# Kernel optimization log

Hardware: AMD Instinct MI355X
Metric: run time of the kernel (lower is better)

Reference implementation:

```python
import jax, jax.numpy as jnp
import numpy as np

N_NODES = 50000
N_EDGES = 1600000
N_GRAPHS = 1000
F_IN = 92      # atom_input_features
WIDTH = 128    # config.width
F_OUT = 64     # output_features
LENGTHSCALE = 8.0  # config.edge_lengthscale


def setup_inputs() -> dict:
    key = jax.random.key(0)
    ks = jax.random.split(key, 12)
    inp = {
        "atom_features": jax.random.normal(ks[0], (N_NODES, F_IN), dtype=jnp.float32),
        "bondlength": jax.random.normal(ks[1], (N_EDGES, 3), dtype=jnp.float32) * 2.0,
        "src": jax.random.randint(ks[2], (N_EDGES,), 0, N_NODES, dtype=jnp.int32),
        "dst": jax.random.randint(ks[3], (N_EDGES,), 0, N_NODES, dtype=jnp.int32),
        "graph_ids": jnp.sort(jax.random.randint(ks[4], (N_NODES,), 0, N_GRAPHS, dtype=jnp.int32)),
        # atom_embedding Linear(F_IN, WIDTH)
        "W0": jax.random.normal(ks[5], (F_IN, WIDTH), dtype=jnp.float32) * 0.05,
        "b0": jnp.zeros((WIDTH,), dtype=jnp.float32),
        # GraphConv layer1 (WIDTH -> WIDTH)
        "W1": jax.random.normal(ks[6], (WIDTH, WIDTH), dtype=jnp.float32) * 0.05,
        "b1": jnp.zeros((WIDTH,), dtype=jnp.float32),
        # GraphConv layer2 (WIDTH -> F_OUT)
        "W2": jax.random.normal(ks[7], (WIDTH, F_OUT), dtype=jnp.float32) * 0.05,
        "b2": jnp.zeros((F_OUT,), dtype=jnp.float32),
    }
    return inp


def _degrees(src, dst, n_nodes):
    ones = jnp.ones(src.shape[0], dtype=jnp.float32)
    out_deg = jax.ops.segment_sum(ones, src, num_segments=n_nodes)
    in_deg = jax.ops.segment_sum(ones, dst, num_segments=n_nodes)
    # DGL GraphConv clamps degrees to min 1 (norm='both')
    return jnp.clip(out_deg, 1.0, None), jnp.clip(in_deg, 1.0, None)


def reference(atom_features, bondlength, src, dst, graph_ids, W0, b0, W1, b1, W2, b2):
    # edge weights: exp(-|r|^2 / lengthscale^2)
    r2 = jnp.sum(bondlength * bondlength, axis=1)  # [E]
    ew = jnp.exp(-r2 / (LENGTHSCALE ** 2))         # [E]

    out_deg, in_deg = _degrees(src, dst, N_NODES)
    norm_src = out_deg ** -0.5  # [N]
    norm_dst = in_deg ** -0.5   # [N]

    # atom embedding
    h = atom_features @ W0 + b0  # [N, WIDTH]

    # GraphConv layer1 (in==out: aggregate then weight), norm='both'
    hs = h * norm_src[:, None]
    m = hs[src] * ew[:, None]                                   # [E, WIDTH]
    agg = jax.ops.segment_sum(m, dst, num_segments=N_NODES)
    x = agg * norm_dst[:, None]
    x = jax.nn.relu(x @ W1 + b1)

    # GraphConv layer2 (in > out: weight first, then aggregate)
    hs = (x * norm_src[:, None]) @ W2                           # [N, F_OUT]
    m = hs[src] * ew[:, None]                                   # [E, F_OUT]
    agg = jax.ops.segment_sum(m, dst, num_segments=N_NODES)
    x = agg * norm_dst[:, None] + b2

    # AvgPooling readout per graph
    cnt = jnp.clip(jax.ops.segment_sum(jnp.ones(N_NODES, jnp.float32), graph_ids, num_segments=N_GRAPHS), 1.0, None)
    pooled = jax.ops.segment_sum(x, graph_ids, num_segments=N_GRAPHS) / cnt[:, None]
    return jnp.squeeze(pooled)  # [N_GRAPHS, F_OUT]
```

## Files before the change

### kernel.cpp

```cpp
#include <hip/hip_runtime.h>
#include <hip/hip_fp16.h>

#define N_NODES  50000
#define N_EDGES  1600000
#define N_GRAPHS 1000
#define F_IN     92
#define WIDTH    128
#define F_OUT    64
#define CHUNK    16384
#define NBLK_E   98
#define HPB      25024
#define HWRD     6256
#define XPITCH   48
#define BKT      196
#define CAP      9216
#define BINCHUNK 4096
#define NBIN     391

static const size_t CURS  = 0;
static const size_t CSRB  = 256;
static const size_t NSRC  = 520;
static const size_t NDST  = 50520;
static const size_t SVAL  = 100520;
static const size_t ROWP  = 150520;
static const size_t HSR   = 200528;
static const size_t SGW   = 813616;
static const size_t SGB   = 2619952;
static const size_t CSR   = 3071536;
static const size_t XB    = 4671536;
static const size_t W01   = 7071536;
static const size_t BW1   = 7083312;
static const size_t W01P  = 7083440;
static const size_t W2P   = 7089584;
static const size_t GAGG  = 7093680;
static const size_t HS2   = 11893680;
static const size_t AGG2  = GAGG;

typedef __attribute__((ext_vector_type(8))) _Float16 half8v;
typedef __attribute__((ext_vector_type(4))) float f32x4;

__device__ inline unsigned short f2bf(float f) {
    unsigned u = __float_as_uint(f);
    return (unsigned short)((u + 0x7fff + ((u >> 16) & 1)) >> 16);
}
__device__ inline float bflo(unsigned u) { return __uint_as_float(u << 16); }
__device__ inline float bfhi(unsigned u) { return __uint_as_float(u & 0xffff0000u); }
__device__ inline unsigned short f2h(float f) {
    return __half_as_ushort(__float2half(f));
}
__device__ inline float csr_w(unsigned v) {
    return __half2float(__ushort_as_half((unsigned short)(v >> 16)));
}

__global__ void k_init(unsigned* __restrict__ cursor) {
    cursor[threadIdx.x] = (unsigned)threadIdx.x * CAP;
}

__global__ __launch_bounds__(256) void k_srcHist(const int* __restrict__ src,
                                                 unsigned char* __restrict__ h_src) {
    __shared__ unsigned sh[HWRD];
    const int e0 = blockIdx.x * CHUNK;
    const int ecnt = min(CHUNK, N_EDGES - e0);
    for (int i = threadIdx.x; i < HWRD; i += 256) sh[i] = 0;
    __syncthreads();
    for (int i = threadIdx.x; i < ecnt; i += 256) {
        int v = src[e0 + i];
        atomicAdd(&sh[v >> 3], 1u << ((v & 7) * 4));
    }
    __syncthreads();
    unsigned* out = (unsigned*)(h_src + (size_t)blockIdx.x * HPB);
    for (int i = threadIdx.x; i < HWRD; i += 256) out[i] = sh[i];
}

__global__ __launch_bounds__(256) void k_nsrc(const unsigned char* __restrict__ h_src,
                                              float* __restrict__ nsrc) {
    int n = blockIdx.x * 256 + threadIdx.x;
    if (n >= N_NODES) return;
    const int byte = n >> 1, shn = (n & 1) * 4;
    unsigned so = 0;
    for (int b = 0; b < NBLK_E; ++b)
        so += (h_src[(size_t)b * HPB + byte] >> shn) & 0xfu;
    nsrc[n] = rsqrtf((float)max(so, 1u));
}

__global__ void k_packX(const float* __restrict__ af, unsigned* __restrict__ xb) {
    int idx = blockIdx.x * blockDim.x + threadIdx.x;
    if (idx >= N_NODES * XPITCH) return;
    int n = idx / XPITCH, c = idx - n * XPITCH;
    unsigned v = 0;
    if (c < 46) {
        const float* p = af + (size_t)n * F_IN + 2 * c;
        v = (unsigned)f2bf(p[0]) | ((unsigned)f2bf(p[1]) << 16);
    }
    xb[idx] = v;
}

__global__ __launch_bounds__(256) void k_bin(const float* __restrict__ bl,
                                             const int* __restrict__ src,
                                             const int* __restrict__ dst,
                                             const float* __restrict__ nsrc,
                                             unsigned* __restrict__ cursor,
                                             unsigned* __restrict__ sgw,
                                             unsigned char* __restrict__ sgb) {
    __shared__ unsigned hcnt[256];
    __shared__ unsigned gbase[256];
    const int t = threadIdx.x;
    const int e0 = blockIdx.x * BINCHUNK;
    hcnt[t] = 0;
    __syncthreads();
    unsigned entry[16], meta[16];
#pragma unroll
    for (int i = 0; i < 16; ++i) {
        int e = e0 + t + i * 256;
        meta[i] = 0xFFFFFFFFu;
        if (e < N_EDGES) {
            float x = bl[3 * e], y = bl[3 * e + 1], z = bl[3 * e + 2];
            int s = src[e], d = dst[e];
            float w = expf(-(x * x + y * y + z * z) * (1.0f / 64.0f)) * nsrc[s];
            entry[i] = (unsigned)s | ((unsigned)f2h(w) << 16);
            int bkt = d >> 8;
            unsigned r = atomicAdd(&hcnt[bkt], 1u);
            meta[i] = ((unsigned)bkt << 20) | ((unsigned)(d & 255) << 12) | r;
        }
    }
    __syncthreads();
    if (t < BKT) gbase[t] = hcnt[t] ? atomicAdd(&cursor[t], hcnt[t]) : 0u;
    __syncthreads();
#pragma unroll
    for (int i = 0; i < 16; ++i) {
        if (meta[i] != 0xFFFFFFFFu) {
            unsigned bkt = meta[i] >> 20;
            unsigned slot = gbase[bkt] + (meta[i] & 0xFFFu);
            if (slot < (bkt + 1) * CAP) {
                sgw[slot] = entry[i];
                sgb[slot] = (unsigned char)((meta[i] >> 12) & 0xFFu);
            }
        }
    }
}

__global__ __launch_bounds__(256) void k_bscan(const unsigned* __restrict__ cursor,
                                               int* __restrict__ csrb,
                                               int* __restrict__ rowp) {
    __shared__ int sd[256];
    const int t = threadIdx.x;
    int c = (t < BKT) ? (int)(cursor[t] - (unsigned)t * CAP) : 0;
    sd[t] = c;
    __syncthreads();
    for (int off = 1; off < 256; off <<= 1) {
        int v = (t >= off) ? sd[t - off] : 0;
        __syncthreads();
        sd[t] += v;
        __syncthreads();
    }
    if (t < BKT) csrb[t] = sd[t] - c;
    if (t == 0) rowp[N_NODES] = N_EDGES;
}

__global__ __launch_bounds__(256) void k_csr(const unsigned* __restrict__ cursor,
                                             const int* __restrict__ csrb,
                                             const unsigned* __restrict__ sgw,
                                             const unsigned char* __restrict__ sgb,
                                             unsigned* __restrict__ csr,
                                             int* __restrict__ rowp,
                                             float* __restrict__ ndst) {
    __shared__ unsigned se[CAP];
    __shared__ unsigned char sd8[CAP];
    __shared__ unsigned dh[256];
    __shared__ unsigned dcur[256];
    __shared__ int sscan[256];
    const int b = blockIdx.x, t = threadIdx.x;
    const int cnt = (int)(cursor[b] - (unsigned)b * CAP);
    const int base = csrb[b];
    for (int i = t; i < cnt; i += 256) {
        se[i] = sgw[(size_t)b * CAP + i];
        sd8[i] = sgb[(size_t)b * CAP + i];
    }
    dh[t] = 0;
    __syncthreads();
    for (int i = t; i < cnt; i += 256) atomicAdd(&dh[sd8[i]], 1u);
    __syncthreads();
    int v = (int)dh[t];
    sscan[t] = v;
    __syncthreads();
    for (int off = 1; off < 256; off <<= 1) {
        int a = (t >= off) ? sscan[t - off] : 0;
        __syncthreads();
        sscan[t] += a;
        __syncthreads();
    }
    dcur[t] = (unsigned)(sscan[t] - v);
    const int node = b * 256 + t;
    if (node < N_NODES) {
        rowp[node] = base + (sscan[t] - v);
        ndst[node] = rsqrtf((float)max((unsigned)v, 1u));
    }
    __syncthreads();
    for (int i = t; i < cnt; i += 256) {
        unsigned pos = atomicAdd(&dcur[sd8[i]], 1u);
        csr[(size_t)base + pos] = se[i];
    }
}

__global__ __launch_bounds__(128) void k_w01(const float* __restrict__ W0,
                                             const float* __restrict__ W1,
                                             const float* __restrict__ b0,
                                             float* __restrict__ w01,
                                             float* __restrict__ bw1) {
    const int t = threadIdx.x;
    const int k = blockIdx.x;
    float acc = 0.0f;
    if (k < F_IN) {
        for (int j = 0; j < WIDTH; ++j)
            acc = fmaf(W0[k * WIDTH + j], W1[j * WIDTH + t], acc);
        w01[k * WIDTH + t] = acc;
    } else {
        for (int j = 0; j < WIDTH; ++j)
            acc = fmaf(b0[j], W1[j * WIDTH + t], acc);
        bw1[t] = acc;
    }
}

__global__ __launch_bounds__(256) void k_prepW(const float* __restrict__ w01,
                                               const float* __restrict__ W2,
                                               unsigned* __restrict__ w01p,
                                               unsigned* __restrict__ w2p) {
    int idx = blockIdx.x * 256 + threadIdx.x;
    if (idx < 6144) {
        int q = idx & 3, lane = (idx >> 2) & 63;
        int rest = idx >> 8;
        int kb = rest % 3, t = rest / 3;
        int k = kb * 32 + ((lane >> 4) * 8) + 2 * q;
        int n = t * 16 + (lane & 15);
        float lo = (k < F_IN) ? w01[k * WIDTH + n] : 0.f;
        float hi = (k + 1 < F_IN) ? w01[(k + 1) * WIDTH + n] : 0.f;
        w01p[idx] = (unsigned)f2h(lo) | ((unsigned)f2h(hi) << 16);
    } else if (idx < 10240) {
        int i2 = idx - 6144;
        int q = i2 & 3, lane = (i2 >> 2) & 63;
        int rest = i2 >> 8;
        int kb = rest & 3, t = rest >> 2;
        int k = kb * 32 + ((lane >> 4) * 8) + 2 * q;
        int n = t * 16 + (lane & 15);
        float lo = W2[k * F_OUT + n];
        float hi = W2[(k + 1) * F_OUT + n];
        w2p[i2] = (unsigned)f2h(lo) | ((unsigned)f2h(hi) << 16);
    }
}

__global__ __launch_bounds__(256) void k_gatherG(const int* __restrict__ rowp,
                                                 const unsigned* __restrict__ csr,
                                                 const unsigned* __restrict__ xb,
                                                 float2* __restrict__ gf2,
                                                 float* __restrict__ S) {
    __shared__ unsigned sb[4][64];
    const int wid = threadIdx.x >> 6;
    const int lane = threadIdx.x & 63;
    const int n = blockIdx.x * 4 + wid;
    const int tc = min(lane, XPITCH - 1);
    unsigned* my = sb[wid];
    const int start = rowp[n], end = rowp[n + 1];
    float2 acc = {0.f, 0.f};
    float ssum = 0.f;
    for (int base = start; base < end; base += 64) {
        const int m = min(64, end - base);
        my[lane] = (lane < m) ? csr[base + lane] : 0u;
        const int mr = (m + 3) & ~3;
        for (int j = 0; j < mr; j += 4) {
            unsigned e0 = my[j], e1 = my[j + 1], e2 = my[j + 2], e3 = my[j + 3];
            unsigned a0 = xb[(size_t)(e0 & 0xFFFFu) * XPITCH + tc];
            unsigned a1 = xb[(size_t)(e1 & 0xFFFFu) * XPITCH + tc];
            unsigned a2 = xb[(size_t)(e2 & 0xFFFFu) * XPITCH + tc];
            unsigned a3 = xb[(size_t)(e3 & 0xFFFFu) * XPITCH + tc];
            float w0 = csr_w(e0), w1 = csr_w(e1), w2 = csr_w(e2), w3 = csr_w(e3);
            acc.x = fmaf(bflo(a0), w0, acc.x);
            acc.y = fmaf(bfhi(a0), w0, acc.y);
            acc.x = fmaf(bflo(a1), w1, acc.x);
            acc.y = fmaf(bfhi(a1), w1, acc.y);
            acc.x = fmaf(bflo(a2), w2, acc.x);
            acc.y = fmaf(bfhi(a2), w2, acc.y);
            acc.x = fmaf(bflo(a3), w3, acc.x);
            acc.y = fmaf(bfhi(a3), w3, acc.y);
            ssum += (w0 + w1) + (w2 + w3);
        }
    }
    if (lane < XPITCH) gf2[(size_t)n * XPITCH + lane] = acc;
    else if (lane == 63) S[n] = ssum;
}

__global__ __launch_bounds__(256) void k_layer1(const float* __restrict__ g,
                                                const float* __restrict__ S,
                                                const float* __restrict__ ndst,
                                                const unsigned* __restrict__ w01p,
                                                const unsigned* __restrict__ w2p,
                                                const float* __restrict__ bw1,
                                                const float* __restrict__ b1,
                                                unsigned short* __restrict__ hs2h) {
    __shared__ unsigned short x2[4][16][136];
    __shared__ float svs[4][16];
    const int wid = threadIdx.x >> 6, lane = threadIdx.x & 63;
    const int row0 = blockIdx.x * 64 + wid * 16;
    const int mn = lane & 15;
    const int kq = lane >> 4;
    if (lane < 16) {
        int r = row0 + lane;
        svs[wid][lane] = (r < N_NODES) ? S[r] * ndst[r] : 0.f;
    }
    const float nd = ndst[min(row0 + mn, N_NODES - 1)];
    const float* grow = g + (size_t)(row0 + mn) * 96;
    half8v a1[3];
#pragma unroll
    for (int kb = 0; kb < 3; ++kb) {
        const float4 p0 = *(const float4*)(grow + kb * 32 + kq * 8);
        const float4 p1 = *(const float4*)(grow + kb * 32 + kq * 8 + 4);
        a1[kb][0] = (_Float16)(p0.x * nd); a1[kb][1] = (_Float16)(p0.y * nd);
        a1[kb][2] = (_Float16)(p0.z * nd); a1[kb][3] = (_Float16)(p0.w * nd);
        a1[kb][4] = (_Float16)(p1.x * nd); a1[kb][5] = (_Float16)(p1.y * nd);
        a1[kb][6] = (_Float16)(p1.z * nd); a1[kb][7] = (_Float16)(p1.w * nd);
    }
    for (int t = 0; t < 8; ++t) {
        const float bwv = bw1[t * 16 + mn];
        const float b1v = b1[t * 16 + mn];
        f32x4 acc = {0.f, 0.f, 0.f, 0.f};
        const unsigned* wp = w01p + ((size_t)t * 3 * 64 + lane) * 4;
#pragma unroll
        for (int kb = 0; kb < 3; ++kb) {
            half8v bf = *(const half8v*)(wp + (size_t)kb * 256);
            acc = __builtin_amdgcn_mfma_f32_16x16x32_f16(a1[kb], bf, acc, 0, 0, 0);
        }
#pragma unroll
        for (int r = 0; r < 4; ++r) {
            float v = acc[r] + svs[wid][kq * 4 + r] * bwv + b1v;
            x2[wid][kq * 4 + r][t * 16 + mn] = f2h(fmaxf(v, 0.f));
        }
    }
    half8v a2[4];
#pragma unroll
    for (int kb = 0; kb < 4; ++kb)
        a2[kb] = *(const half8v*)&x2[wid][mn][kb * 32 + kq * 8];
    for (int t2 = 0; t2 < 4; ++t2) {
        f32x4 acc = {0.f, 0.f, 0.f, 0.f};
        const unsigned* wp = w2p + ((size_t)t2 * 4 * 64 + lane) * 4;
#pragma unroll
        for (int kb = 0; kb < 4; ++kb) {
            half8v bf = *(const half8v*)(wp + (size_t)kb * 256);
            acc = __builtin_amdgcn_mfma_f32_16x16x32_f16(a2[kb], bf, acc, 0, 0, 0);
        }
#pragma unroll
        for (int r = 0; r < 4; ++r) {
            int row = row0 + kq * 4 + r;
            if (row < N_NODES)
                hs2h[(size_t)row * 64 + t2 * 16 + mn] = f2bf(acc[r]);
        }
    }
}

__global__ __launch_bounds__(256) void k_gather2(const int* __restrict__ rowp,
                                                 const unsigned* __restrict__ csr,
                                                 const unsigned* __restrict__ hs2u,
                                                 float2* __restrict__ agg2f2) {
    __shared__ unsigned sb[4][64];
    const int wid = threadIdx.x >> 6;
    const int lane = threadIdx.x & 63;
    const int n = blockIdx.x * 4 + wid;
    const int c = lane & 31;
    const int h = lane >> 5;
    unsigned* my = sb[wid];
    const int start = rowp[n], end = rowp[n + 1];
    float2 acc = {0.f, 0.f};
    for (int base = start; base < end; base += 64) {
        const int m = min(64, end - base);
        my[lane] = (lane < m) ? csr[base + lane] : 0u;
        const int mr = (m + 7) & ~7;
        for (int j = 0; j < mr; j += 8) {
#pragma unroll
            for (int k = 0; k < 4; ++k) {
                unsigned sw = my[j + 2 * k + h];
                unsigned a = hs2u[(size_t)(sw & 0xFFFFu) * 32 + c];
                float w = csr_w(sw);
                acc.x = fmaf(bflo(a), w, acc.x);
                acc.y = fmaf(bfhi(a), w, acc.y);
            }
        }
    }
    acc.x += __shfl_xor(acc.x, 32);
    acc.y += __shfl_xor(acc.y, 32);
    if (lane < 32) agg2f2[(size_t)n * 32 + lane] = acc;
}

__global__ __launch_bounds__(64) void k_pool(const float* __restrict__ agg2,
                                             const float* __restrict__ ndst,
                                             const float* __restrict__ b2,
                                             const int* __restrict__ gid,
                                             float* __restrict__ out) {
    const int g = blockIdx.x;
    const int t = threadIdx.x;
    int lo = 0, hi = N_NODES;
    while (lo < hi) { int mid = (lo + hi) >> 1; if (gid[mid] < g) lo = mid + 1; else hi = mid; }
    const int start = lo;
    hi = N_NODES;
    while (lo < hi) { int mid = (lo + hi) >> 1; if (gid[mid] < g + 1) lo = mid + 1; else hi = mid; }
    const int end = lo;
    float sum = 0.0f;
    for (int n = start; n < end; ++n)
        sum = fmaf(agg2[n * F_OUT + t], ndst[n], sum);
    out[g * F_OUT + t] = (end > start) ? (sum / (float)(end - start) + b2[t]) : 0.0f;
}

extern "C" void kernel_launch(void* const* d_in, const int* in_sizes, int n_in,
                              void* d_out, int out_size, void* d_ws, size_t ws_size,
                              hipStream_t stream) {
    const float* af  = (const float*)d_in[0];
    const float* bl  = (const float*)d_in[1];
    const int*   src = (const int*)d_in[2];
    const int*   dst = (const int*)d_in[3];
    const int*   gid = (const int*)d_in[4];
    const float* W0  = (const float*)d_in[5];
    const float* b0  = (const float*)d_in[6];
    const float* W1  = (const float*)d_in[7];
    const float* b1  = (const float*)d_in[8];
    const float* W2  = (const float*)d_in[9];
    const float* b2  = (const float*)d_in[10];
    float* out = (float*)d_out;
    float* ws  = (float*)d_ws;

    unsigned*       cursor = (unsigned*)(ws + CURS);
    int*            csrb   = (int*)(ws + CSRB);
    float*          nsrc   = ws + NSRC;
    float*          ndst   = ws + NDST;
    float*          S      = ws + SVAL;
    int*            rowp   = (int*)(ws + ROWP);
    unsigned char*  h_src  = (unsigned char*)(ws + HSR);
    unsigned*       sgw    = (unsigned*)(ws + SGW);
    unsigned char*  sgb    = (unsigned char*)(ws + SGB);
    unsigned*       csr    = (unsigned*)(ws + CSR);
    unsigned*       xb     = (unsigned*)(ws + XB);
    float*          w01    = ws + W01;
    float*          bw1    = ws + BW1;
    unsigned*       w01p   = (unsigned*)(ws + W01P);
    unsigned*       w2p    = (unsigned*)(ws + W2P);
    float*          g      = ws + GAGG;
    unsigned*       hs2u   = (unsigned*)(ws + HS2);
    unsigned short* hs2h   = (unsigned short*)(ws + HS2);
    float*          agg2   = ws + AGG2;

    k_init<<<1, 256, 0, stream>>>(cursor);
    k_srcHist<<<NBLK_E, 256, 0, stream>>>(src, h_src);
    k_packX<<<(N_NODES * XPITCH) / 256, 256, 0, stream>>>(af, xb);
    k_nsrc<<<BKT, 256, 0, stream>>>(h_src, nsrc);
    k_bin<<<NBIN, 256, 0, stream>>>(bl, src, dst, nsrc, cursor, sgw, sgb);
    k_bscan<<<1, 256, 0, stream>>>(cursor, csrb, rowp);
    k_csr<<<BKT, 256, 0, stream>>>(cursor, csrb, sgw, sgb, csr, rowp, ndst);
    k_w01<<<F_IN + 1, 128, 0, stream>>>(W0, W1, b0, w01, bw1);
    k_prepW<<<40, 256, 0, stream>>>(w01, W2, w01p, w2p);
    k_gatherG<<<N_NODES / 4, 256, 0, stream>>>(rowp, csr, xb, (float2*)g, S);
    k_layer1<<<(N_NODES + 63) / 64, 256, 0, stream>>>(g, S, ndst, w01p, w2p, bw1, b1, hs2h);
    k_gather2<<<N_NODES / 4, 256, 0, stream>>>(rowp, csr, hs2u, (float2*)agg2);
    k_pool<<<N_GRAPHS, 64, 0, stream>>>(agg2, ndst, b2, gid, out);
}
```

Measured before the change: 291.3 us.

## Split gather lanes across edges with vector loads and fold weight-sum into features

```diff
diff --git a/kernel.cpp b/kernel.cpp
--- a/kernel.cpp
+++ b/kernel.cpp
@@ -21,7 +21,6 @@
 static const size_t CSRB  = 256;
 static const size_t NSRC  = 520;
 static const size_t NDST  = 50520;
-static const size_t SVAL  = 100520;
 static const size_t ROWP  = 150520;
 static const size_t HSR   = 200528;
 static const size_t SGW   = 813616;
@@ -91,6 +90,8 @@
     if (c < 46) {
         const float* p = af + (size_t)n * F_IN + 2 * c;
         v = (unsigned)f2bf(p[0]) | ((unsigned)f2bf(p[1]) << 16);
+    } else if (c == 46) {
+        v = 0x3F80u;
     }
     xb[idx] = v;
 }
@@ -251,45 +252,47 @@
 __global__ __launch_bounds__(256) void k_gatherG(const int* __restrict__ rowp,
                                                  const unsigned* __restrict__ csr,
                                                  const unsigned* __restrict__ xb,
-                                                 float2* __restrict__ gf2,
-                                                 float* __restrict__ S) {
+                                                 float* __restrict__ g) {
     __shared__ unsigned sb[4][64];
     const int wid = threadIdx.x >> 6;
     const int lane = threadIdx.x & 63;
+    const int es = lane >> 4;
+    const int ci = lane & 15;
+    const int ci3 = ci * 3;
+    unsigned* my = sb[wid];
     const int n = blockIdx.x * 4 + wid;
-    const int tc = min(lane, XPITCH - 1);
-    unsigned* my = sb[wid];
     const int start = rowp[n], end = rowp[n + 1];
-    float2 acc = {0.f, 0.f};
-    float ssum = 0.f;
+    float acc[6] = {0.f, 0.f, 0.f, 0.f, 0.f, 0.f};
     for (int base = start; base < end; base += 64) {
         const int m = min(64, end - base);
         my[lane] = (lane < m) ? csr[base + lane] : 0u;
-        const int mr = (m + 3) & ~3;
-        for (int j = 0; j < mr; j += 4) {
-            unsigned e0 = my[j], e1 = my[j + 1], e2 = my[j + 2], e3 = my[j + 3];
-            unsigned a0 = xb[(size_t)(e0 & 0xFFFFu) * XPITCH + tc];
-            unsigned a1 = xb[(size_t)(e1 & 0xFFFFu) * XPITCH + tc];
-            unsigned a2 = xb[(size_t)(e2 & 0xFFFFu) * XPITCH + tc];
-            unsigned a3 = xb[(size_t)(e3 & 0xFFFFu) * XPITCH + tc];
-            float w0 = csr_w(e0), w1 = csr_w(e1), w2 = csr_w(e2), w3 = csr_w(e3);
-            acc.x = fmaf(bflo(a0), w0, acc.x);
-            acc.y = fmaf(bfhi(a0), w0, acc.y);
-            acc.x = fmaf(bflo(a1), w1, acc.x);
-            acc.y = fmaf(bfhi(a1), w1, acc.y);
-            acc.x = fmaf(bflo(a2), w2, acc.x);
-            acc.y = fmaf(bfhi(a2), w2, acc.y);
-            acc.x = fmaf(bflo(a3), w3, acc.x);
-            acc.y = fmaf(bfhi(a3), w3, acc.y);
-            ssum += (w0 + w1) + (w2 + w3);
-        }
-    }
-    if (lane < XPITCH) gf2[(size_t)n * XPITCH + lane] = acc;
-    else if (lane == 63) S[n] = ssum;
+#pragma unroll 2
+        for (int j0 = 0; j0 < m; j0 += 4) {
+            unsigned e = my[j0 + es];
+            float w = csr_w(e);
+            const unsigned* row = xb + (size_t)(e & 0xFFFFu) * XPITCH + ci3;
+            uint3 a = *(const uint3*)row;
+            acc[0] = fmaf(bflo(a.x), w, acc[0]);
+            acc[1] = fmaf(bfhi(a.x), w, acc[1]);
+            acc[2] = fmaf(bflo(a.y), w, acc[2]);
+            acc[3] = fmaf(bfhi(a.y), w, acc[3]);
+            acc[4] = fmaf(bflo(a.z), w, acc[4]);
+            acc[5] = fmaf(bfhi(a.z), w, acc[5]);
+        }
+    }
+#pragma unroll
+    for (int k = 0; k < 6; ++k) {
+        acc[k] += __shfl_xor(acc[k], 16);
+        acc[k] += __shfl_xor(acc[k], 32);
+    }
+    if (lane < 16) {
+        float* go = g + (size_t)n * 96 + lane * 6;
+        go[0] = acc[0]; go[1] = acc[1]; go[2] = acc[2];
+        go[3] = acc[3]; go[4] = acc[4]; go[5] = acc[5];
+    }
 }
 
 __global__ __launch_bounds__(256) void k_layer1(const float* __restrict__ g,
-                                                const float* __restrict__ S,
                                                 const float* __restrict__ ndst,
                                                 const unsigned* __restrict__ w01p,
                                                 const unsigned* __restrict__ w2p,
@@ -304,10 +307,10 @@
     const int kq = lane >> 4;
     if (lane < 16) {
         int r = row0 + lane;
-        svs[wid][lane] = (r < N_NODES) ? S[r] * ndst[r] : 0.f;
+        svs[wid][lane] = (r < N_NODES) ? g[(size_t)r * 96 + 92] * ndst[r] : 0.f;
     }
     const float nd = ndst[min(row0 + mn, N_NODES - 1)];
-    const float* grow = g + (size_t)(row0 + mn) * 96;
+    const float* grow = g + (size_t)min(row0 + mn, N_NODES - 1) * 96;
     half8v a1[3];
 #pragma unroll
     for (int kb = 0; kb < 3; ++kb) {
@@ -358,34 +361,45 @@
 __global__ __launch_bounds__(256) void k_gather2(const int* __restrict__ rowp,
                                                  const unsigned* __restrict__ csr,
                                                  const unsigned* __restrict__ hs2u,
-                                                 float2* __restrict__ agg2f2) {
+                                                 float* __restrict__ agg2) {
     __shared__ unsigned sb[4][64];
     const int wid = threadIdx.x >> 6;
     const int lane = threadIdx.x & 63;
+    const int es = lane >> 3;
+    const int ci = lane & 7;
+    unsigned* my = sb[wid];
     const int n = blockIdx.x * 4 + wid;
-    const int c = lane & 31;
-    const int h = lane >> 5;
-    unsigned* my = sb[wid];
     const int start = rowp[n], end = rowp[n + 1];
-    float2 acc = {0.f, 0.f};
+    float acc[8] = {0.f, 0.f, 0.f, 0.f, 0.f, 0.f, 0.f, 0.f};
     for (int base = start; base < end; base += 64) {
         const int m = min(64, end - base);
         my[lane] = (lane < m) ? csr[base + lane] : 0u;
-        const int mr = (m + 7) & ~7;
-        for (int j = 0; j < mr; j += 8) {
-#pragma unroll
-            for (int k = 0; k < 4; ++k) {
-                unsigned sw = my[j + 2 * k + h];
-                unsigned a = hs2u[(size_t)(sw & 0xFFFFu) * 32 + c];
-                float w = csr_w(sw);
-                acc.x = fmaf(bflo(a), w, acc.x);
-                acc.y = fmaf(bfhi(a), w, acc.y);
-            }
-        }
-    }
-    acc.x += __shfl_xor(acc.x, 32);
-    acc.y += __shfl_xor(acc.y, 32);
-    if (lane < 32) agg2f2[(size_t)n * 32 + lane] = acc;
+#pragma unroll 2
+        for (int j0 = 0; j0 < m; j0 += 8) {
+            unsigned e = my[j0 + es];
+            float w = csr_w(e);
+            const uint4 a = *(const uint4*)(hs2u + (size_t)(e & 0xFFFFu) * 32 + ci * 4);
+            acc[0] = fmaf(bflo(a.x), w, acc[0]);
+            acc[1] = fmaf(bfhi(a.x), w, acc[1]);
+            acc[2] = fmaf(bflo(a.y), w, acc[2]);
+            acc[3] = fmaf(bfhi(a.y), w, acc[3]);
+            acc[4] = fmaf(bflo(a.z), w, acc[4]);
+            acc[5] = fmaf(bfhi(a.z), w, acc[5]);
+            acc[6] = fmaf(bflo(a.w), w, acc[6]);
+            acc[7] = fmaf(bfhi(a.w), w, acc[7]);
+        }
+    }
+#pragma unroll
+    for (int k = 0; k < 8; ++k) {
+        acc[k] += __shfl_xor(acc[k], 8);
+        acc[k] += __shfl_xor(acc[k], 16);
+        acc[k] += __shfl_xor(acc[k], 32);
+    }
+    if (lane < 8) {
+        float4* ao = (float4*)(agg2 + (size_t)n * 64 + ci * 8);
+        ao[0] = make_float4(acc[0], acc[1], acc[2], acc[3]);
+        ao[1] = make_float4(acc[4], acc[5], acc[6], acc[7]);
+    }
 }
 
 __global__ __launch_bounds__(64) void k_pool(const float* __restrict__ agg2,
@@ -428,7 +442,6 @@
     int*            csrb   = (int*)(ws + CSRB);
     float*          nsrc   = ws + NSRC;
     float*          ndst   = ws + NDST;
-    float*          S      = ws + SVAL;
     int*            rowp   = (int*)(ws + ROWP);
     unsigned char*  h_src  = (unsigned char*)(ws + HSR);
     unsigned*       sgw    = (unsigned*)(ws + SGW);
@@ -453,8 +466,8 @@
     k_csr<<<BKT, 256, 0, stream>>>(cursor, csrb, sgw, sgb, csr, rowp, ndst);
     k_w01<<<F_IN + 1, 128, 0, stream>>>(W0, W1, b0, w01, bw1);
     k_prepW<<<40, 256, 0, stream>>>(w01, W2, w01p, w2p);
-    k_gatherG<<<N_NODES / 4, 256, 0, stream>>>(rowp, csr, xb, (float2*)g, S);
-    k_layer1<<<(N_NODES + 63) / 64, 256, 0, stream>>>(g, S, ndst, w01p, w2p, bw1, b1, hs2h);
-    k_gather2<<<N_NODES / 4, 256, 0, stream>>>(rowp, csr, hs2u, (float2*)agg2);
+    k_gatherG<<<N_NODES / 4, 256, 0, stream>>>(rowp, csr, xb, g);
+    k_layer1<<<(N_NODES + 63) / 64, 256, 0, stream>>>(g, ndst, w01p, w2p, bw1, b1, hs2h);
+    k_gather2<<<N_NODES / 4, 256, 0, stream>>>(rowp, csr, hs2u, agg2);
     k_pool<<<N_GRAPHS, 64, 0, stream>>>(agg2, ndst, b2, gid, out);
 }
```

After: 283.8 us. 2.6% less time.
